# Kernel optimization log

Hardware: AMD Instinct MI355X
Metric: run time of the kernel (lower is better)

Reference implementation:

```python
import jax, jax.numpy as jnp
import numpy as np

NUM_HEADS = 12


def setup_inputs() -> dict:
    key = jax.random.key(0)
    k1, k2, k3 = jax.random.split(key, 3)
    B, T, N, D = 8, 8, 196, 768
    x = jax.random.normal(k1, (B, T * N, D), dtype=jnp.float32)
    w_qkv = jax.random.normal(k2, (D, 3 * D), dtype=jnp.float32) * 0.02
    w_proj = jax.random.normal(k3, (D, D), dtype=jnp.float32) * 0.02
    b_proj = jnp.zeros((D,), dtype=jnp.float32)
    return {"x": x, "T": T, "N": N, "w_qkv": w_qkv, "w_proj": w_proj, "b_proj": b_proj}


def reference(x, T, N, w_qkv, w_proj, b_proj):
    B, TN, D = x.shape
    H = NUM_HEADS
    hd = D // H
    scale = hd ** -0.5
    # qkv projection: (B, TN, 3, H, hd)
    qkv = (x @ w_qkv).reshape(B, TN, 3, H, hd)
    # -> (3, B, H, T, N, hd)
    qkv = jnp.transpose(qkv, (2, 0, 3, 1, 4)).reshape(3, B, H, T, N, hd)
    q, k, v = qkv[0], qkv[1], qkv[2]

    # Temporal branch: mean-pool over spatial axis N (keepdim -> length-1 attn axis)
    q_t = q.mean(axis=3, keepdims=True)            # (B,H,T,1,hd)
    k_t = k.mean(axis=3, keepdims=True)            # (B,H,T,1,hd)
    v_t = v.mean(axis=3, keepdims=True)            # (B,H,T,1,hd)
    attn_t = jnp.einsum('bhtqd,bhtkd->bhtqk', q_t, k_t) * scale  # (B,H,T,1,1)
    attn_t = jax.nn.softmax(attn_t, axis=-1)
    x_t = jnp.einsum('bhtqk,bhtkd->bhtqd', attn_t, v_t)[:, :, :, 0]  # (B,H,T,hd)

    # Spatial branch: full attention within each frame
    attn_s = jnp.einsum('bhtnd,bhtmd->bhtnm', q, k) * scale  # (B,H,T,N,N)
    attn_s = jax.nn.softmax(attn_s, axis=-1)
    x_s = jnp.einsum('bhtnm,bhtmd->bhtnd', attn_s, v)        # (B,H,T,N,hd)

    # Combine: broadcast temporal result over spatial positions, add
    out = x_s + x_t[:, :, :, None, :]                        # (B,H,T,N,hd)
    out = out.reshape(B, H, T * N, hd)
    out = jnp.transpose(out, (0, 2, 1, 3)).reshape(B * T * N, D)
    return out @ w_proj + b_proj
```

## Files before the change

### kernel.cpp

```cpp
#include <hip/hip_runtime.h>
#include <math.h>

#define BB 8
#define TT 8
#define NN 196
#define DD 768
#define HH 12
#define HD 64
#define TN (TT * NN)
#define MM (BB * TN)
#define D3 (3 * DD)

typedef _Float16 f16;
typedef _Float16 f16x8 __attribute__((ext_vector_type(8)));
typedef _Float16 f16x4 __attribute__((ext_vector_type(4)));
typedef float f32x4 __attribute__((ext_vector_type(4)));
typedef unsigned int u32;

#define GLDS16(gp, lp)                                                        \
  __builtin_amdgcn_global_load_lds(                                           \
      (const __attribute__((address_space(1))) u32*)(gp),                     \
      (__attribute__((address_space(3))) u32*)(lp), 16, 0, 0)

#define MFMA16(a, b, c) __builtin_amdgcn_mfma_f32_16x16x32_f16(a, b, c, 0, 0, 0)

__global__ __launch_bounds__(256) void gemm_f16nt(
    const f16* __restrict__ A, const f16* __restrict__ Bt,
    float* __restrict__ C32, f16* __restrict__ C16, int K, int Ncol,
    const float* __restrict__ bias) {
  __shared__ f16 As[128 * 32];
  __shared__ f16 Bs[128 * 32];

  const int tid = threadIdx.x;
  const int lane = tid & 63;
  const int wave = tid >> 6;
  const int wy = wave >> 1, wx = wave & 1;
  const int bm = blockIdx.y * 128;
  const int bn = blockIdx.x * 128;

  const int ci0 = tid;
  const int ci1 = tid + 256;
  const int r0 = ci0 >> 2, c0 = (ci0 & 3) ^ ((r0 >> 1) & 3);
  const int r1 = ci1 >> 2, c1 = (ci1 & 3) ^ ((r1 >> 1) & 3);

  const f16* a0p = A + (size_t)(bm + r0) * K + c0 * 8;
  const f16* a1p = A + (size_t)(bm + r1) * K + c1 * 8;
  const f16* b0p = Bt + (size_t)(bn + r0) * K + c0 * 8;
  const f16* b1p = Bt + (size_t)(bn + r1) * K + c1 * 8;

  f32x4 acc[4][4];
#pragma unroll
  for (int i = 0; i < 4; i++)
#pragma unroll
    for (int j = 0; j < 4; j++) acc[i][j] = (f32x4)0.0f;

  const int fr = lane & 15;
  const int fqp = (((lane >> 4) ^ ((fr >> 1) & 3)) * 8);

  for (int kt = 0; kt < K; kt += 32) {
    GLDS16(a0p + kt, &As[ci0 * 8]);
    GLDS16(a1p + kt, &As[ci1 * 8]);
    GLDS16(b0p + kt, &Bs[ci0 * 8]);
    GLDS16(b1p + kt, &Bs[ci1 * 8]);
    __syncthreads();

    f16x8 af[4], bf[4];
#pragma unroll
    for (int mi = 0; mi < 4; mi++)
      af[mi] = *(const f16x8*)&As[(wy * 64 + mi * 16 + fr) * 32 + fqp];
#pragma unroll
    for (int ni = 0; ni < 4; ni++)
      bf[ni] = *(const f16x8*)&Bs[(wx * 64 + ni * 16 + fr) * 32 + fqp];

#pragma unroll
    for (int mi = 0; mi < 4; mi++)
#pragma unroll
      for (int ni = 0; ni < 4; ni++)
        acc[mi][ni] = MFMA16(af[mi], bf[ni], acc[mi][ni]);

    __syncthreads();
  }

#pragma unroll
  for (int mi = 0; mi < 4; mi++) {
    const int row0 = bm + wy * 64 + mi * 16 + (lane >> 4) * 4;
#pragma unroll
    for (int ni = 0; ni < 4; ni++) {
      const int col = bn + wx * 64 + ni * 16 + (lane & 15);
      float bv = (bias != nullptr) ? bias[col] : 0.0f;
      if (C16 != nullptr) {
#pragma unroll
        for (int r = 0; r < 4; r++)
          C16[(size_t)(row0 + r) * Ncol + col] = (f16)(acc[mi][ni][r] + bv);
      } else {
#pragma unroll
        for (int r = 0; r < 4; r++)
          C32[(size_t)(row0 + r) * Ncol + col] = acc[mi][ni][r] + bv;
      }
    }
  }
}

__global__ __launch_bounds__(256) void conv_f32_to_f16(
    const float* __restrict__ in, f16* __restrict__ out, int n4) {
  int i = blockIdx.x * blockDim.x + threadIdx.x;
  const int stride = gridDim.x * blockDim.x;
  for (; i < n4; i += stride) {
    float4 f = ((const float4*)in)[i];
    f16x4 h;
    h[0] = (f16)f.x;
    h[1] = (f16)f.y;
    h[2] = (f16)f.z;
    h[3] = (f16)f.w;
    ((f16x4*)out)[i] = h;
  }
}

__global__ __launch_bounds__(256) void transpose_f32_to_f16(
    const float* __restrict__ W, f16* __restrict__ Wt, int K, int Ncol) {
  __shared__ float tileS[32][33];
  const int k0 = blockIdx.y * 32, n0 = blockIdx.x * 32;
  const int tx = threadIdx.x & 31, ty = threadIdx.x >> 5;
#pragma unroll
  for (int i = 0; i < 4; i++)
    tileS[ty + i * 8][tx] = W[(size_t)(k0 + ty + i * 8) * Ncol + n0 + tx];
  __syncthreads();
#pragma unroll
  for (int i = 0; i < 4; i++)
    Wt[(size_t)(n0 + ty + i * 8) * K + k0 + tx] = (f16)tileS[tx][ty + i * 8];
}

#define VSTR 232

__global__ __launch_bounds__(512, 4) void attn_mfma(
    const f16* __restrict__ qkv, f16* __restrict__ out) {
  __shared__ f16 KS[196 * 64];
  __shared__ f16 VS[64 * VSTR];
  __shared__ __align__(16) f16 PS[8 * 16 * 40];
  __shared__ float vmean[64];
  float* red = (float*)PS;

  const int bi = blockIdx.x;
  const int t = bi % TT;
  const int h = (bi / TT) % HH;
  const int b = bi / (TT * HH);
  const int tok0 = b * TN + t * NN;

  const int tid = threadIdx.x;
  const int lane = tid & 63;
  const int wave = tid >> 6;
  const int m = lane & 15;
  const int q = lane >> 4;

#pragma unroll
  for (int it = 0; it < 4; it++) {
    int idx = tid + it * 512;
    if (idx < 196 * 8) {
      int key = idx >> 3, c = idx & 7;
      f16x8 val = *(const f16x8*)(qkv + (size_t)(tok0 + key) * D3 + DD +
                                  h * HD + c * 8);
      *(f16x8*)&KS[key * 64 + ((c ^ (key & 7)) * 8)] = val;
    }
  }

  for (int idx = tid; idx < 64 * 9; idx += 512) {
    int d = idx / 9, c = idx % 9;
    *(f16x4*)&VS[d * VSTR + 196 + c * 4] = (f16x4){0, 0, 0, 0};
  }

  const int vd = tid & 63;
  const int kb = tid >> 6;
  float vpart = 0.0f;
  if (kb < 7) {
#pragma unroll
    for (int it = 0; it < 7; it++) {
      int k0 = kb * 28 + it * 4;
      f16x4 pk;
#pragma unroll
      for (int j = 0; j < 4; j++) {
        f16 v = qkv[(size_t)(tok0 + k0 + j) * D3 + 2 * DD + h * HD + vd];
        pk[j] = v;
        vpart += (float)v;
      }
      *(f16x4*)&VS[vd * VSTR + k0] = pk;
    }
  }
  red[tid] = vpart;
  __syncthreads();
  if (tid < 64) {
    float s = 0.0f;
#pragma unroll
    for (int g = 0; g < 8; g++) s += red[tid + 64 * g];
    vmean[tid] = s * (1.0f / (float)NN);
  }
  __syncthreads();

  f16* PSw = &PS[wave * 640];

  for (int qt = wave; qt < 13; qt += 8) {
    const int q0 = qt * 16;
    int qrow = q0 + m;
    if (qrow > NN - 1) qrow = NN - 1;
    const f16* qbase = qkv + (size_t)(tok0 + qrow) * D3 + h * HD;
    f16x8 aq0 = *(const f16x8*)(qbase + q * 8);
    f16x8 aq1 = *(const f16x8*)(qbase + 32 + q * 8);

    f32x4 o0 = (f32x4)0.0f, o1 = (f32x4)0.0f, o2 = (f32x4)0.0f,
          o3 = (f32x4)0.0f;
    float l[4] = {0.0f, 0.0f, 0.0f, 0.0f};

    for (int ch = 0; ch < 7; ch++) {
      const int keyA = ch * 32 + m;
      const int keyB = keyA + 16;
      const int kA = keyA > 195 ? 195 : keyA;
      const int kB = keyB > 195 ? 195 : keyB;
      const int swA = kA & 7, swB = kB & 7;
      f16x8 b00 = *(const f16x8*)&KS[kA * 64 + ((q ^ swA) * 8)];
      f16x8 b01 = *(const f16x8*)&KS[kA * 64 + (((q + 4) ^ swA) * 8)];
      f16x8 b10 = *(const f16x8*)&KS[kB * 64 + ((q ^ swB) * 8)];
      f16x8 b11 = *(const f16x8*)&KS[kB * 64 + (((q + 4) ^ swB) * 8)];
      f32x4 z = (f32x4)0.0f;
      f32x4 s0 = MFMA16(aq0, b00, z);
      s0 = MFMA16(aq1, b01, s0);
      f32x4 s1 = MFMA16(aq0, b10, z);
      s1 = MFMA16(aq1, b11, s1);

      const bool v0 = keyA < NN;
      const bool v1 = keyB < NN;
#pragma unroll
      for (int r = 0; r < 4; r++) {
        float p0 = v0 ? __expf(s0[r] * 0.125f) : 0.0f;
        float p1 = v1 ? __expf(s1[r] * 0.125f) : 0.0f;
        l[r] += p0 + p1;
        PSw[(q * 4 + r) * 40 + m] = (f16)p0;
        PSw[(q * 4 + r) * 40 + 16 + m] = (f16)p1;
      }
      f16x8 pa = *(const f16x8*)&PSw[m * 40 + q * 8];
      f16x8 bv0 = *(const f16x8*)&VS[(0 * 16 + m) * VSTR + ch * 32 + q * 8];
      f16x8 bv1 = *(const f16x8*)&VS[(1 * 16 + m) * VSTR + ch * 32 + q * 8];
      f16x8 bv2 = *(const f16x8*)&VS[(2 * 16 + m) * VSTR + ch * 32 + q * 8];
      f16x8 bv3 = *(const f16x8*)&VS[(3 * 16 + m) * VSTR + ch * 32 + q * 8];
      o0 = MFMA16(pa, bv0, o0);
      o1 = MFMA16(pa, bv1, o1);
      o2 = MFMA16(pa, bv2, o2);
      o3 = MFMA16(pa, bv3, o3);
    }

#pragma unroll
    for (int r = 0; r < 4; r++) {
      float s = l[r];
      s += __shfl_xor(s, 1);
      s += __shfl_xor(s, 2);
      s += __shfl_xor(s, 4);
      s += __shfl_xor(s, 8);
      l[r] = 1.0f / s;
    }

#pragma unroll
    for (int r = 0; r < 4; r++) {
      const int query = q0 + q * 4 + r;
      if (query < NN) {
        f16* orow = out + (size_t)(tok0 + query) * DD + h * HD;
        orow[m] = (f16)(o0[r] * l[r] + vmean[m]);
        orow[16 + m] = (f16)(o1[r] * l[r] + vmean[16 + m]);
        orow[32 + m] = (f16)(o2[r] * l[r] + vmean[32 + m]);
        orow[48 + m] = (f16)(o3[r] * l[r] + vmean[48 + m]);
      }
    }
  }
}

extern "C" void kernel_launch(void* const* d_in, const int* in_sizes, int n_in,
                              void* d_out, int out_size, void* d_ws,
                              size_t ws_size, hipStream_t stream) {
  (void)in_sizes;
  (void)n_in;
  (void)out_size;
  (void)ws_size;
  const float* x      = (const float*)d_in[0];
  const float* w_qkv  = (const float*)d_in[3];
  const float* w_proj = (const float*)d_in[4];
  const float* b_proj = (const float*)d_in[5];
  float* out = (float*)d_out;

  char* ws = (char*)d_ws;
  f16* qkvh = (f16*)ws;
  f16* xh = (f16*)(ws + (size_t)MM * D3 * 2);
  f16* wqkvT = xh + (size_t)MM * DD;
  f16* wprojT = wqkvT + (size_t)D3 * DD;

  conv_f32_to_f16<<<2048, 256, 0, stream>>>(x, xh, MM * DD / 4);
  transpose_f32_to_f16<<<dim3(D3 / 32, DD / 32), 256, 0, stream>>>(w_qkv,
                                                                   wqkvT, DD, D3);
  transpose_f32_to_f16<<<dim3(DD / 32, DD / 32), 256, 0, stream>>>(w_proj,
                                                                   wprojT, DD, DD);
  gemm_f16nt<<<dim3(D3 / 128, MM / 128), 256, 0, stream>>>(
      xh, wqkvT, nullptr, qkvh, DD, D3, nullptr);
  attn_mfma<<<BB * HH * TT, 512, 0, stream>>>(qkvh, xh);
  gemm_f16nt<<<dim3(DD / 128, MM / 128), 256, 0, stream>>>(
      xh, wprojT, out, nullptr, DD, DD, b_proj);
}
```

Measured before the change: 239.5 us.

## Write QKV in per-frame-head layout and double GEMM K-tile to 64

```diff
diff --git a/kernel.cpp b/kernel.cpp
--- a/kernel.cpp
+++ b/kernel.cpp
@@ -27,9 +27,9 @@
 __global__ __launch_bounds__(256) void gemm_f16nt(
     const f16* __restrict__ A, const f16* __restrict__ Bt,
     float* __restrict__ C32, f16* __restrict__ C16, int K, int Ncol,
-    const float* __restrict__ bias) {
-  __shared__ f16 As[128 * 32];
-  __shared__ f16 Bs[128 * 32];
+    const float* __restrict__ bias, int mode) {
+  __shared__ f16 As[128 * 64];
+  __shared__ f16 Bs[128 * 64];
 
   const int tid = threadIdx.x;
   const int lane = tid & 63;
@@ -38,15 +38,16 @@
   const int bm = blockIdx.y * 128;
   const int bn = blockIdx.x * 128;
 
-  const int ci0 = tid;
-  const int ci1 = tid + 256;
-  const int r0 = ci0 >> 2, c0 = (ci0 & 3) ^ ((r0 >> 1) & 3);
-  const int r1 = ci1 >> 2, c1 = (ci1 & 3) ^ ((r1 >> 1) & 3);
-
-  const f16* a0p = A + (size_t)(bm + r0) * K + c0 * 8;
-  const f16* a1p = A + (size_t)(bm + r1) * K + c1 * 8;
-  const f16* b0p = Bt + (size_t)(bn + r0) * K + c0 * 8;
-  const f16* b1p = Bt + (size_t)(bn + r1) * K + c1 * 8;
+  const f16* aP[4];
+  const f16* bP[4];
+#pragma unroll
+  for (int it = 0; it < 4; it++) {
+    int ci = tid + it * 256;
+    int r = ci >> 3;
+    int c = (ci & 7) ^ (r & 7);
+    aP[it] = A + (size_t)(bm + r) * K + c * 8;
+    bP[it] = Bt + (size_t)(bn + r) * K + c * 8;
+  }
 
   f32x4 acc[4][4];
 #pragma unroll
@@ -55,47 +56,69 @@
     for (int j = 0; j < 4; j++) acc[i][j] = (f32x4)0.0f;
 
   const int fr = lane & 15;
-  const int fqp = (((lane >> 4) ^ ((fr >> 1) & 3)) * 8);
-
-  for (int kt = 0; kt < K; kt += 32) {
-    GLDS16(a0p + kt, &As[ci0 * 8]);
-    GLDS16(a1p + kt, &As[ci1 * 8]);
-    GLDS16(b0p + kt, &Bs[ci0 * 8]);
-    GLDS16(b1p + kt, &Bs[ci1 * 8]);
+  const int q = lane >> 4;
+  const int sw = fr & 7;
+
+  for (int kt = 0; kt < K; kt += 64) {
+#pragma unroll
+    for (int it = 0; it < 4; it++) {
+      GLDS16(aP[it] + kt, &As[(tid + it * 256) * 8]);
+      GLDS16(bP[it] + kt, &Bs[(tid + it * 256) * 8]);
+    }
     __syncthreads();
 
-    f16x8 af[4], bf[4];
-#pragma unroll
-    for (int mi = 0; mi < 4; mi++)
-      af[mi] = *(const f16x8*)&As[(wy * 64 + mi * 16 + fr) * 32 + fqp];
-#pragma unroll
-    for (int ni = 0; ni < 4; ni++)
-      bf[ni] = *(const f16x8*)&Bs[(wx * 64 + ni * 16 + fr) * 32 + fqp];
-
-#pragma unroll
-    for (int mi = 0; mi < 4; mi++)
+#pragma unroll
+    for (int kk = 0; kk < 2; kk++) {
+      const int lc = ((kk * 4 + q) ^ sw) * 8;
+      f16x8 af[4], bf[4];
+#pragma unroll
+      for (int mi = 0; mi < 4; mi++)
+        af[mi] = *(const f16x8*)&As[(wy * 64 + mi * 16 + fr) * 64 + lc];
 #pragma unroll
       for (int ni = 0; ni < 4; ni++)
-        acc[mi][ni] = MFMA16(af[mi], bf[ni], acc[mi][ni]);
-
+        bf[ni] = *(const f16x8*)&Bs[(wx * 64 + ni * 16 + fr) * 64 + lc];
+
+#pragma unroll
+      for (int mi = 0; mi < 4; mi++)
+#pragma unroll
+        for (int ni = 0; ni < 4; ni++)
+          acc[mi][ni] = MFMA16(af[mi], bf[ni], acc[mi][ni]);
+    }
     __syncthreads();
   }
 
-#pragma unroll
-  for (int mi = 0; mi < 4; mi++) {
-    const int row0 = bm + wy * 64 + mi * 16 + (lane >> 4) * 4;
-#pragma unroll
-    for (int ni = 0; ni < 4; ni++) {
-      const int col = bn + wx * 64 + ni * 16 + (lane & 15);
-      float bv = (bias != nullptr) ? bias[col] : 0.0f;
-      if (C16 != nullptr) {
-#pragma unroll
-        for (int r = 0; r < 4; r++)
-          C16[(size_t)(row0 + r) * Ncol + col] = (f16)(acc[mi][ni][r] + bv);
-      } else {
+  if (mode == 0) {
+#pragma unroll
+    for (int mi = 0; mi < 4; mi++) {
+      const int row0 = bm + wy * 64 + mi * 16 + (lane >> 4) * 4;
+#pragma unroll
+      for (int ni = 0; ni < 4; ni++) {
+        const int col = bn + wx * 64 + ni * 16 + (lane & 15);
+        float bv = (bias != nullptr) ? bias[col] : 0.0f;
 #pragma unroll
         for (int r = 0; r < 4; r++)
           C32[(size_t)(row0 + r) * Ncol + col] = acc[mi][ni][r] + bv;
+      }
+    }
+  } else {
+#pragma unroll
+    for (int mi = 0; mi < 4; mi++) {
+      const int row0 = bm + wy * 64 + mi * 16 + (lane >> 4) * 4;
+#pragma unroll
+      for (int r = 0; r < 4; r++) {
+        const int token = row0 + r;
+        const int f = token / NN;
+        const int n = token - f * NN;
+        f16* fb = C16 + ((size_t)f * (HH * 3) * NN) * 64 + n * 64;
+#pragma unroll
+        for (int ni = 0; ni < 4; ni++) {
+          const int col = bn + wx * 64 + ni * 16 + (lane & 15);
+          const int qt = col / DD;
+          const int rem = col - qt * DD;
+          const int hh = rem >> 6;
+          const int d = rem & 63;
+          fb[(size_t)(hh * 3 + qt) * NN * 64 + d] = (f16)acc[mi][ni][r];
+        }
       }
     }
   }
@@ -144,7 +167,12 @@
   const int t = bi % TT;
   const int h = (bi / TT) % HH;
   const int b = bi / (TT * HH);
-  const int tok0 = b * TN + t * NN;
+  const int frame = b * TT + t;
+  const int tok0 = frame * NN;
+
+  const f16* Qb = qkv + (size_t)(frame * HH + h) * 3 * NN * 64;
+  const f16* Kb = Qb + NN * 64;
+  const f16* Vb = Qb + 2 * NN * 64;
 
   const int tid = threadIdx.x;
   const int lane = tid & 63;
@@ -153,14 +181,17 @@
   const int q = lane >> 4;
 
 #pragma unroll
-  for (int it = 0; it < 4; it++) {
-    int idx = tid + it * 512;
-    if (idx < 196 * 8) {
-      int key = idx >> 3, c = idx & 7;
-      f16x8 val = *(const f16x8*)(qkv + (size_t)(tok0 + key) * D3 + DD +
-                                  h * HD + c * 8);
-      *(f16x8*)&KS[key * 64 + ((c ^ (key & 7)) * 8)] = val;
-    }
+  for (int it = 0; it < 3; it++) {
+    int chunk = tid + it * 512;
+    int row = chunk >> 3, pc = chunk & 7;
+    int c = pc ^ (row & 7);
+    GLDS16(Kb + row * 64 + c * 8, &KS[chunk * 8]);
+  }
+  if (tid < 32) {
+    int chunk = 1536 + tid;
+    int row = chunk >> 3, pc = chunk & 7;
+    int c = pc ^ (row & 7);
+    *(f16x8*)&KS[chunk * 8] = *(const f16x8*)(Kb + row * 64 + c * 8);
   }
 
   for (int idx = tid; idx < 64 * 9; idx += 512) {
@@ -178,7 +209,7 @@
       f16x4 pk;
 #pragma unroll
       for (int j = 0; j < 4; j++) {
-        f16 v = qkv[(size_t)(tok0 + k0 + j) * D3 + 2 * DD + h * HD + vd];
+        f16 v = Vb[(k0 + j) * 64 + vd];
         pk[j] = v;
         vpart += (float)v;
       }
@@ -201,7 +232,7 @@
     const int q0 = qt * 16;
     int qrow = q0 + m;
     if (qrow > NN - 1) qrow = NN - 1;
-    const f16* qbase = qkv + (size_t)(tok0 + qrow) * D3 + h * HD;
+    const f16* qbase = Qb + qrow * 64;
     f16x8 aq0 = *(const f16x8*)(qbase + q * 8);
     f16x8 aq1 = *(const f16x8*)(qbase + 32 + q * 8);
 
@@ -295,8 +326,8 @@
   transpose_f32_to_f16<<<dim3(DD / 32, DD / 32), 256, 0, stream>>>(w_proj,
                                                                    wprojT, DD, DD);
   gemm_f16nt<<<dim3(D3 / 128, MM / 128), 256, 0, stream>>>(
-      xh, wqkvT, nullptr, qkvh, DD, D3, nullptr);
+      xh, wqkvT, nullptr, qkvh, DD, D3, nullptr, 1);
   attn_mfma<<<BB * HH * TT, 512, 0, stream>>>(qkvh, xh);
   gemm_f16nt<<<dim3(DD / 128, MM / 128), 256, 0, stream>>>(
-      xh, wprojT, out, nullptr, DD, DD, b_proj);
-}
+      xh, wprojT, out, nullptr, DD, DD, b_proj, 0);
+}
```

Result: faster. 234.1 us (-2.2%).
